# Optimization experiments

Measured on AMD Instinct MI355X. Metric: run time of the kernel, lower is better.

The kernel has to match this reference:

```python
import jax, jax.numpy as jnp
import numpy as np
from jax import lax

SIGMA = 3.0
AP_CUT = 15


def _gauss_kernel(sigma, truncate=4.0):
    r = int(truncate * sigma + 0.5)
    x = np.arange(-r, r + 1, dtype=np.float32)
    k = np.exp(-0.5 * (x / sigma) ** 2)
    return jnp.asarray(k / k.sum()), r

KERN, RAD = _gauss_kernel(SIGMA)


def _smooth(f):
    """Separable Gaussian smoothing; circular on y (DV), replicate on x (AP).
    f: [..., Y, X] -> same shape."""
    lead = f.shape[:-2]
    Y, X = f.shape[-2:]
    g = f.reshape((-1, 1, Y, X))
    g = jnp.pad(g, ((0, 0), (0, 0), (RAD, RAD), (0, 0)), mode='wrap')
    g = jnp.pad(g, ((0, 0), (0, 0), (0, 0), (RAD, RAD)), mode='edge')
    ky = KERN.reshape(1, 1, -1, 1)
    kx = KERN.reshape(1, 1, 1, -1)
    g = lax.conv_general_dilated(g, ky, (1, 1), 'VALID')
    g = lax.conv_general_dilated(g, kx, (1, 1), 'VALID')
    return g.reshape(lead + (Y, X))


def _gradient(f):
    """Covariant gradient: Gaussian smooth then central differences.
    Returns [..., Y, X, 2] with index 0 = d/dy (circular), 1 = d/dx (replicate)."""
    g = _smooth(f)
    dy = 0.5 * (jnp.roll(g, -1, axis=-2) - jnp.roll(g, 1, axis=-2))
    gp = jnp.pad(g, [(0, 0)] * (g.ndim - 1) + [(1, 1)], mode='edge')
    dx = 0.5 * (gp[..., 2:] - gp[..., :-2])
    return jnp.stack([dy, dx], axis=-1)


def _postprocess(f):
    f = f.at[..., :AP_CUT].set(0.0)
    f = f.at[..., -AP_CUT:].set(0.0)
    return _smooth(f)


def setup_inputs() -> dict:
    key = jax.random.key(0)
    k1, k2 = jax.random.split(key)
    Y, X = 1024, 2048
    y = 0.1 * jax.random.normal(k1, (5, Y, X), dtype=jnp.float32)
    v = 0.1 * jax.random.normal(k2, (2, Y, X), dtype=jnp.float32)
    return {"y": y, "v": v}


def reference(y, v):
    Y, X = y.shape[-2:]
    # InputProcessor.transform: split state into 2x2 tensor m and scalar s
    m = y[:4].reshape(2, 2, Y, X)
    s = y[4]

    # get_velocity: left-right symmetrization (flip DV axis, negate y-component)
    v_lr = jnp.flip(v, axis=-2)
    v_lr = v_lr.at[0].multiply(-1.0)
    v = 0.5 * (v + v_lr)

    d1_m = _gradient(m)          # [2,2,Y,X,2]
    d1_s = _gradient(s)          # [Y,X,2]
    d1_v = _gradient(v)          # [2,Y,X,2]

    sdot = -jnp.einsum('iyx,yxi->yx', v, d1_s)

    T = jnp.transpose(d1_v, (0, 3, 1, 2))       # iyxj -> ijyx
    Tt = jnp.transpose(T, (1, 0, 2, 3))
    O = -0.5 * (T - Tt)                         # vorticity
    E = 0.5 * (T + Tt)                          # strain rate

    lhs = jnp.einsum('kyx,ijyxk->ijyx', v, d1_m)
    lhs = lhs + jnp.einsum('ikyx,kjyx->ijyx', O, m)
    lhs = lhs - jnp.einsum('ikyx,kjyx->ijyx', m, O)

    # rhs_eCad reaction terms
    trm = jnp.einsum('kkyx->yx', m)
    trE = jnp.einsum('kkyx->yx', E)
    gamma_dv = jnp.array([[1.0, 0.0], [0.0, 0.0]], dtype=y.dtype)[..., None, None]
    rhs = -(0.11 - 0.099 * s) * m
    rhs = rhs + (0.767 + 0.055 * s) * m * trE
    rhs = rhs + (0.732 - 0.59 * s) * trm * m
    rhs = rhs + (0.069 - 0.048 * s) * trm * gamma_dv

    mdot = _postprocess(-lhs + rhs)
    sdot = _postprocess(sdot)

    # inverse_transform: stack back into 5-channel state derivative
    return jnp.concatenate([mdot.reshape(4, Y, X), sdot[None]], axis=0)
```

## Files before the change

### kernel.cpp

```cpp
#include <hip/hip_runtime.h>
#include <math.h>

#define Y_ 1024
#define X_ 2048
#define YX_ (Y_*X_)
#define RAD_ 12
#define NT_ 25
#define APC_ 15

struct W25 { float w[NT_]; };

__global__ __launch_bounds__(256) void ksmooth_y7(
    const float* __restrict__ yin, const float* __restrict__ vin,
    float* __restrict__ out, W25 W)
{
  const int z  = blockIdx.z;
  const int y0 = blockIdx.y * 8;
  const int xo = (blockIdx.x * 256 + threadIdx.x) * 4;

  float4 acc[8];
#pragma unroll
  for (int j = 0; j < 8; ++j) acc[j] = make_float4(0.f, 0.f, 0.f, 0.f);

#pragma unroll
  for (int t = 0; t < 32; ++t) {
    int r = y0 - RAD_ + t;
    if (r < 0)    r += Y_;
    if (r >= Y_)  r -= Y_;
    float4 val;
    if (z < 5) {
      val = *(const float4*)(yin + z * YX_ + r * X_ + xo);
    } else {
      const int   c   = z - 5;
      const float sgn = (c == 0) ? -1.f : 1.f;
      float4 a = *(const float4*)(vin + c * YX_ + r * X_ + xo);
      float4 b = *(const float4*)(vin + c * YX_ + (Y_ - 1 - r) * X_ + xo);
      val.x = 0.5f * (a.x + sgn * b.x);
      val.y = 0.5f * (a.y + sgn * b.y);
      val.z = 0.5f * (a.z + sgn * b.z);
      val.w = 0.5f * (a.w + sgn * b.w);
    }
#pragma unroll
    for (int j = 0; j < 8; ++j) {
      const int k = t - j;
      if (k >= 0 && k < NT_) {
        const float wk = W.w[k];
        acc[j].x += wk * val.x; acc[j].y += wk * val.y;
        acc[j].z += wk * val.z; acc[j].w += wk * val.w;
      }
    }
  }
#pragma unroll
  for (int j = 0; j < 8; ++j)
    *(float4*)(out + z * YX_ + (y0 + j) * X_ + xo) = acc[j];
}

__global__ __launch_bounds__(256) void ksmooth_y(
    const float* __restrict__ in, float* __restrict__ out, W25 W)
{
  const int z  = blockIdx.z;
  const int y0 = blockIdx.y * 8;
  const int xo = (blockIdx.x * 256 + threadIdx.x) * 4;

  float4 acc[8];
#pragma unroll
  for (int j = 0; j < 8; ++j) acc[j] = make_float4(0.f, 0.f, 0.f, 0.f);

#pragma unroll
  for (int t = 0; t < 32; ++t) {
    int r = y0 - RAD_ + t;
    if (r < 0)    r += Y_;
    if (r >= Y_)  r -= Y_;
    float4 val = *(const float4*)(in + z * YX_ + r * X_ + xo);
#pragma unroll
    for (int j = 0; j < 8; ++j) {
      const int k = t - j;
      if (k >= 0 && k < NT_) {
        const float wk = W.w[k];
        acc[j].x += wk * val.x; acc[j].y += wk * val.y;
        acc[j].z += wk * val.z; acc[j].w += wk * val.w;
      }
    }
  }
#pragma unroll
  for (int j = 0; j < 8; ++j)
    *(float4*)(out + z * YX_ + (y0 + j) * X_ + xo) = acc[j];
}

__global__ __launch_bounds__(256) void ksmooth_x(
    const float* __restrict__ in, float* __restrict__ out, W25 W)
{
  const int z  = blockIdx.z;
  const int yy = blockIdx.y;
  const int x0 = (blockIdx.x * 256 + threadIdx.x) * 4;
  const float* row = in + z * YX_ + yy * X_;

  float buf[28];
  if (x0 >= RAD_ && x0 + 4 + RAD_ <= X_) {
#pragma unroll
    for (int i = 0; i < 7; ++i) {
      float4 t = *(const float4*)(row + x0 - RAD_ + 4 * i);
      buf[4*i+0] = t.x; buf[4*i+1] = t.y; buf[4*i+2] = t.z; buf[4*i+3] = t.w;
    }
  } else {
#pragma unroll
    for (int i = 0; i < 28; ++i) {
      int xx = x0 - RAD_ + i;
      xx = xx < 0 ? 0 : (xx > X_ - 1 ? X_ - 1 : xx);
      buf[i] = row[xx];
    }
  }
  float a0 = 0.f, a1 = 0.f, a2 = 0.f, a3 = 0.f;
#pragma unroll
  for (int t = 0; t < NT_; ++t) {
    const float wk = W.w[t];
    a0 += wk * buf[t + 0];
    a1 += wk * buf[t + 1];
    a2 += wk * buf[t + 2];
    a3 += wk * buf[t + 3];
  }
  *(float4*)(out + z * YX_ + yy * X_ + x0) = make_float4(a0, a1, a2, a3);
}

__global__ __launch_bounds__(256) void kpoint(
    const float* __restrict__ gs,
    const float* __restrict__ yin,
    const float* __restrict__ vin,
    float* __restrict__ out)
{
  const int yy = blockIdx.y;
  const int x0 = (blockIdx.x * 256 + threadIdx.x) * 4;
  const int yu = (yy + 1) & (Y_ - 1);
  const int yd = (yy - 1 + Y_) & (Y_ - 1);

  float dYg[7][4], dXg[7][4];
#pragma unroll
  for (int c = 0; c < 7; ++c) {
    const float* base = gs + c * YX_;
    float4 cc = *(const float4*)(base + yy * X_ + x0);
    float4 uu = *(const float4*)(base + yu * X_ + x0);
    float4 dd = *(const float4*)(base + yd * X_ + x0);
    float L  = (x0 == 0)       ? cc.x : base[yy * X_ + x0 - 1];
    float Rr = (x0 + 4 >= X_)  ? cc.w : base[yy * X_ + x0 + 4];
    dYg[c][0] = 0.5f * (uu.x - dd.x);
    dYg[c][1] = 0.5f * (uu.y - dd.y);
    dYg[c][2] = 0.5f * (uu.z - dd.z);
    dYg[c][3] = 0.5f * (uu.w - dd.w);
    dXg[c][0] = 0.5f * (cc.y - L);
    dXg[c][1] = 0.5f * (cc.z - cc.x);
    dXg[c][2] = 0.5f * (cc.w - cc.y);
    dXg[c][3] = 0.5f * (Rr - cc.z);
  }

  float rm[5][4];
#pragma unroll
  for (int zc = 0; zc < 5; ++zc) {
    float4 t = *(const float4*)(yin + zc * YX_ + yy * X_ + x0);
    rm[zc][0] = t.x; rm[zc][1] = t.y; rm[zc][2] = t.z; rm[zc][3] = t.w;
  }
  float vs0[4], vs1[4];
  {
    float4 a = *(const float4*)(vin + 0 * YX_ + yy * X_ + x0);
    float4 b = *(const float4*)(vin + 0 * YX_ + (Y_ - 1 - yy) * X_ + x0);
    vs0[0] = 0.5f * (a.x - b.x); vs0[1] = 0.5f * (a.y - b.y);
    vs0[2] = 0.5f * (a.z - b.z); vs0[3] = 0.5f * (a.w - b.w);
    float4 c = *(const float4*)(vin + 1 * YX_ + yy * X_ + x0);
    float4 d = *(const float4*)(vin + 1 * YX_ + (Y_ - 1 - yy) * X_ + x0);
    vs1[0] = 0.5f * (c.x + d.x); vs1[1] = 0.5f * (c.y + d.y);
    vs1[2] = 0.5f * (c.z + d.z); vs1[3] = 0.5f * (c.w + d.w);
  }

  float o[5][4];
#pragma unroll
  for (int j = 0; j < 4; ++j) {
    const float m00r = rm[0][j], m01r = rm[1][j], m10r = rm[2][j], m11r = rm[3][j];
    const float sr   = rm[4][j];
    const float v0   = vs0[j], v1 = vs1[j];

    const float w_  = -0.5f * (dXg[5][j] - dYg[6][j]);
    const float trE = dYg[5][j] + dXg[6][j];
    const float trm = m00r + m11r;

    const float adv00 = v0 * dYg[0][j] + v1 * dXg[0][j];
    const float adv01 = v0 * dYg[1][j] + v1 * dXg[1][j];
    const float adv10 = v0 * dYg[2][j] + v1 * dXg[2][j];
    const float adv11 = v0 * dYg[3][j] + v1 * dXg[3][j];

    const float lhs00 = adv00 + w_ * (m10r + m01r);
    const float lhs01 = adv01 + w_ * (m11r - m00r);
    const float lhs10 = adv10 + w_ * (m11r - m00r);
    const float lhs11 = adv11 - w_ * (m01r + m10r);

    const float f  = -(0.11f - 0.099f * sr)
                   + (0.767f + 0.055f * sr) * trE
                   + (0.732f - 0.59f  * sr) * trm;
    const float cd = (0.069f - 0.048f * sr) * trm;

    const float sd = -(v0 * dYg[4][j] + v1 * dXg[4][j]);

    const int   xg   = x0 + j;
    const float mask = (xg < APC_ || xg >= X_ - APC_) ? 0.f : 1.f;
    o[0][j] = mask * (f * m00r + cd - lhs00);
    o[1][j] = mask * (f * m01r      - lhs01);
    o[2][j] = mask * (f * m10r      - lhs10);
    o[3][j] = mask * (f * m11r      - lhs11);
    o[4][j] = mask * sd;
  }
#pragma unroll
  for (int zc = 0; zc < 5; ++zc)
    *(float4*)(out + zc * YX_ + yy * X_ + x0) =
        make_float4(o[zc][0], o[zc][1], o[zc][2], o[zc][3]);
}

extern "C" void kernel_launch(void* const* d_in, const int* in_sizes, int n_in,
                              void* d_out, int out_size, void* d_ws, size_t ws_size,
                              hipStream_t stream)
{
  const float* yin = (const float*)d_in[0];
  const float* vin = (const float*)d_in[1];
  float* out = (float*)d_out;

  float* wsA = (float*)d_ws;
  float* wsB = wsA + 7 * (size_t)YX_;

  W25 W;
  double wd[NT_], s = 0.0;
  for (int i = 0; i < NT_; ++i) {
    double x = i - RAD_;
    wd[i] = exp(-0.5 * (x / 3.0) * (x / 3.0));
    s += wd[i];
  }
  for (int i = 0; i < NT_; ++i) W.w[i] = (float)(wd[i] / s);

  ksmooth_y7<<<dim3(2, 128, 7), 256, 0, stream>>>(yin, vin, wsA, W);
  ksmooth_x <<<dim3(2, 1024, 7), 256, 0, stream>>>(wsA, wsB, W);
  kpoint    <<<dim3(2, 1024, 1), 256, 0, stream>>>(wsB, yin, vin, wsA);
  ksmooth_y <<<dim3(2, 128, 5), 256, 0, stream>>>(wsA, wsB, W);
  ksmooth_x <<<dim3(2, 1024, 5), 256, 0, stream>>>(wsB, out, W);
}
```

Measured before the change: 239.8 us.

## Fuse x-smoothing into gradient and postprocess kernels, folding derivative into filter

Removes the separate x-direction smoothing passes. The x-gradient becomes a single 27-tap derivative-of-Gaussian filter, and the y-gradient applies the x-Gaussian to central differences inside the pointwise kernel. The final smoothing does the x-filter on the fly for each input row before the y-accumulation. The y-smoothing kernel now produces 16 rows per thread instead of 8. Two intermediate 7- and 5-channel round trips through global memory go away, at the cost of redundant x-filter arithmetic per row. Edge columns are zeroed early, which relies on the AP cut masking the replicate-boundary region.

```diff
diff --git a/kernel.cpp b/kernel.cpp
--- a/kernel.cpp
+++ b/kernel.cpp
@@ -6,27 +6,28 @@
 #define YX_ (Y_*X_)
 #define RAD_ 12
 #define NT_ 25
+#define ND_ 27
 #define APC_ 15
+#define PAD_ 16
 
 struct W25 { float w[NT_]; };
+struct D27 { float d[ND_]; };
 
 __global__ __launch_bounds__(256) void ksmooth_y7(
     const float* __restrict__ yin, const float* __restrict__ vin,
     float* __restrict__ out, W25 W)
 {
   const int z  = blockIdx.z;
-  const int y0 = blockIdx.y * 8;
+  const int y0 = blockIdx.y * 16;
   const int xo = (blockIdx.x * 256 + threadIdx.x) * 4;
 
-  float4 acc[8];
-#pragma unroll
-  for (int j = 0; j < 8; ++j) acc[j] = make_float4(0.f, 0.f, 0.f, 0.f);
-
-#pragma unroll
-  for (int t = 0; t < 32; ++t) {
-    int r = y0 - RAD_ + t;
-    if (r < 0)    r += Y_;
-    if (r >= Y_)  r -= Y_;
+  float4 acc[16];
+#pragma unroll
+  for (int j = 0; j < 16; ++j) acc[j] = make_float4(0.f, 0.f, 0.f, 0.f);
+
+#pragma unroll
+  for (int t = 0; t < 40; ++t) {
+    const int r = (y0 - RAD_ + t + Y_) & (Y_ - 1);
     float4 val;
     if (z < 5) {
       val = *(const float4*)(yin + z * YX_ + r * X_ + xo);
@@ -41,7 +42,7 @@
       val.w = 0.5f * (a.w + sgn * b.w);
     }
 #pragma unroll
-    for (int j = 0; j < 8; ++j) {
+    for (int j = 0; j < 16; ++j) {
       const int k = t - j;
       if (k >= 0 && k < NT_) {
         const float wk = W.w[k];
@@ -51,105 +52,66 @@
     }
   }
 #pragma unroll
-  for (int j = 0; j < 8; ++j)
+  for (int j = 0; j < 16; ++j)
     *(float4*)(out + z * YX_ + (y0 + j) * X_ + xo) = acc[j];
 }
 
-__global__ __launch_bounds__(256) void ksmooth_y(
-    const float* __restrict__ in, float* __restrict__ out, W25 W)
-{
-  const int z  = blockIdx.z;
-  const int y0 = blockIdx.y * 8;
-  const int xo = (blockIdx.x * 256 + threadIdx.x) * 4;
-
-  float4 acc[8];
-#pragma unroll
-  for (int j = 0; j < 8; ++j) acc[j] = make_float4(0.f, 0.f, 0.f, 0.f);
-
-#pragma unroll
-  for (int t = 0; t < 32; ++t) {
-    int r = y0 - RAD_ + t;
-    if (r < 0)    r += Y_;
-    if (r >= Y_)  r -= Y_;
-    float4 val = *(const float4*)(in + z * YX_ + r * X_ + xo);
-#pragma unroll
-    for (int j = 0; j < 8; ++j) {
-      const int k = t - j;
-      if (k >= 0 && k < NT_) {
-        const float wk = W.w[k];
-        acc[j].x += wk * val.x; acc[j].y += wk * val.y;
-        acc[j].z += wk * val.z; acc[j].w += wk * val.w;
-      }
-    }
-  }
-#pragma unroll
-  for (int j = 0; j < 8; ++j)
-    *(float4*)(out + z * YX_ + (y0 + j) * X_ + xo) = acc[j];
-}
-
-__global__ __launch_bounds__(256) void ksmooth_x(
-    const float* __restrict__ in, float* __restrict__ out, W25 W)
-{
-  const int z  = blockIdx.z;
+__global__ __launch_bounds__(256) void kgradpoint(
+    const float* __restrict__ gY,
+    const float* __restrict__ yin,
+    const float* __restrict__ vin,
+    float* __restrict__ out,
+    W25 W, D27 D)
+{
   const int yy = blockIdx.y;
   const int x0 = (blockIdx.x * 256 + threadIdx.x) * 4;
-  const float* row = in + z * YX_ + yy * X_;
-
-  float buf[28];
-  if (x0 >= RAD_ && x0 + 4 + RAD_ <= X_) {
-#pragma unroll
-    for (int i = 0; i < 7; ++i) {
-      float4 t = *(const float4*)(row + x0 - RAD_ + 4 * i);
-      buf[4*i+0] = t.x; buf[4*i+1] = t.y; buf[4*i+2] = t.z; buf[4*i+3] = t.w;
-    }
-  } else {
-#pragma unroll
-    for (int i = 0; i < 28; ++i) {
-      int xx = x0 - RAD_ + i;
-      xx = xx < 0 ? 0 : (xx > X_ - 1 ? X_ - 1 : xx);
-      buf[i] = row[xx];
-    }
-  }
-  float a0 = 0.f, a1 = 0.f, a2 = 0.f, a3 = 0.f;
-#pragma unroll
-  for (int t = 0; t < NT_; ++t) {
-    const float wk = W.w[t];
-    a0 += wk * buf[t + 0];
-    a1 += wk * buf[t + 1];
-    a2 += wk * buf[t + 2];
-    a3 += wk * buf[t + 3];
-  }
-  *(float4*)(out + z * YX_ + yy * X_ + x0) = make_float4(a0, a1, a2, a3);
-}
-
-__global__ __launch_bounds__(256) void kpoint(
-    const float* __restrict__ gs,
-    const float* __restrict__ yin,
-    const float* __restrict__ vin,
-    float* __restrict__ out)
-{
-  const int yy = blockIdx.y;
-  const int x0 = (blockIdx.x * 256 + threadIdx.x) * 4;
+
+  if (x0 < RAD_ || x0 > X_ - PAD_) {
+#pragma unroll
+    for (int zc = 0; zc < 5; ++zc)
+      *(float4*)(out + zc * YX_ + yy * X_ + x0) = make_float4(0.f, 0.f, 0.f, 0.f);
+    return;
+  }
+
   const int yu = (yy + 1) & (Y_ - 1);
   const int yd = (yy - 1 + Y_) & (Y_ - 1);
 
   float dYg[7][4], dXg[7][4];
 #pragma unroll
   for (int c = 0; c < 7; ++c) {
-    const float* base = gs + c * YX_;
-    float4 cc = *(const float4*)(base + yy * X_ + x0);
-    float4 uu = *(const float4*)(base + yu * X_ + x0);
-    float4 dd = *(const float4*)(base + yd * X_ + x0);
-    float L  = (x0 == 0)       ? cc.x : base[yy * X_ + x0 - 1];
-    float Rr = (x0 + 4 >= X_)  ? cc.w : base[yy * X_ + x0 + 4];
-    dYg[c][0] = 0.5f * (uu.x - dd.x);
-    dYg[c][1] = 0.5f * (uu.y - dd.y);
-    dYg[c][2] = 0.5f * (uu.z - dd.z);
-    dYg[c][3] = 0.5f * (uu.w - dd.w);
-    dXg[c][0] = 0.5f * (cc.y - L);
-    dXg[c][1] = 0.5f * (cc.z - cc.x);
-    dXg[c][2] = 0.5f * (cc.w - cc.y);
-    dXg[c][3] = 0.5f * (Rr - cc.z);
+    const float* rc = gY + c * YX_ + yy * X_;
+    const float* ru = gY + c * YX_ + yu * X_;
+    const float* rd = gY + c * YX_ + yd * X_;
+
+    float wb[36];
+#pragma unroll
+    for (int i = 0; i < 9; ++i) {
+      float4 t = *(const float4*)(rc + x0 - 16 + 4 * i);
+      wb[4*i+0] = t.x; wb[4*i+1] = t.y; wb[4*i+2] = t.z; wb[4*i+3] = t.w;
+    }
+#pragma unroll
+    for (int j = 0; j < 4; ++j) {
+      float s = 0.f;
+#pragma unroll
+      for (int t = 0; t < ND_; ++t) s += D.d[t] * wb[3 + j + t];
+      dXg[c][j] = s;
+    }
+
+    float db[28];
+#pragma unroll
+    for (int i = 0; i < 7; ++i) {
+      float4 u = *(const float4*)(ru + x0 - 12 + 4 * i);
+      float4 d = *(const float4*)(rd + x0 - 12 + 4 * i);
+      db[4*i+0] = 0.5f * (u.x - d.x); db[4*i+1] = 0.5f * (u.y - d.y);
+      db[4*i+2] = 0.5f * (u.z - d.z); db[4*i+3] = 0.5f * (u.w - d.w);
+    }
+#pragma unroll
+    for (int j = 0; j < 4; ++j) {
+      float s = 0.f;
+#pragma unroll
+      for (int t = 0; t < NT_; ++t) s += W.w[t] * db[j + t];
+      dYg[c][j] = s;
+    }
   }
 
   float rm[5][4];
@@ -181,21 +143,15 @@
     const float trE = dYg[5][j] + dXg[6][j];
     const float trm = m00r + m11r;
 
-    const float adv00 = v0 * dYg[0][j] + v1 * dXg[0][j];
-    const float adv01 = v0 * dYg[1][j] + v1 * dXg[1][j];
-    const float adv10 = v0 * dYg[2][j] + v1 * dXg[2][j];
-    const float adv11 = v0 * dYg[3][j] + v1 * dXg[3][j];
-
-    const float lhs00 = adv00 + w_ * (m10r + m01r);
-    const float lhs01 = adv01 + w_ * (m11r - m00r);
-    const float lhs10 = adv10 + w_ * (m11r - m00r);
-    const float lhs11 = adv11 - w_ * (m01r + m10r);
+    const float lhs00 = v0 * dYg[0][j] + v1 * dXg[0][j] + w_ * (m10r + m01r);
+    const float lhs01 = v0 * dYg[1][j] + v1 * dXg[1][j] + w_ * (m11r - m00r);
+    const float lhs10 = v0 * dYg[2][j] + v1 * dXg[2][j] + w_ * (m11r - m00r);
+    const float lhs11 = v0 * dYg[3][j] + v1 * dXg[3][j] - w_ * (m01r + m10r);
 
     const float f  = -(0.11f - 0.099f * sr)
                    + (0.767f + 0.055f * sr) * trE
                    + (0.732f - 0.59f  * sr) * trm;
     const float cd = (0.069f - 0.048f * sr) * trm;
-
     const float sd = -(v0 * dYg[4][j] + v1 * dXg[4][j]);
 
     const int   xg   = x0 + j;
@@ -212,6 +168,61 @@
         make_float4(o[zc][0], o[zc][1], o[zc][2], o[zc][3]);
 }
 
+__global__ __launch_bounds__(256) void kpost(
+    const float* __restrict__ B, float* __restrict__ out, W25 W)
+{
+  const int z  = blockIdx.z;
+  const int y0 = blockIdx.y * 16;
+  const int xo = (blockIdx.x * 256 + threadIdx.x) * 4;
+  const bool fast = (xo >= RAD_ && xo <= X_ - PAD_);
+
+  float4 acc[16];
+#pragma unroll
+  for (int j = 0; j < 16; ++j) acc[j] = make_float4(0.f, 0.f, 0.f, 0.f);
+
+  for (int t = 0; t < 40; ++t) {
+    const int r = (y0 - RAD_ + t + Y_) & (Y_ - 1);
+    const float* row = B + z * YX_ + r * X_;
+    float xb[28];
+    if (fast) {
+#pragma unroll
+      for (int i = 0; i < 7; ++i) {
+        float4 v = *(const float4*)(row + xo - 12 + 4 * i);
+        xb[4*i+0] = v.x; xb[4*i+1] = v.y; xb[4*i+2] = v.z; xb[4*i+3] = v.w;
+      }
+    } else {
+#pragma unroll
+      for (int i = 0; i < 28; ++i) {
+        const int xx = xo - 12 + i;
+        xb[i] = (xx >= 0 && xx < X_) ? row[xx] : 0.f;
+      }
+    }
+    float4 xs;
+    {
+      float a0 = 0.f, a1 = 0.f, a2 = 0.f, a3 = 0.f;
+#pragma unroll
+      for (int k = 0; k < NT_; ++k) {
+        const float wk = W.w[k];
+        a0 += wk * xb[k + 0]; a1 += wk * xb[k + 1];
+        a2 += wk * xb[k + 2]; a3 += wk * xb[k + 3];
+      }
+      xs = make_float4(a0, a1, a2, a3);
+    }
+#pragma unroll
+    for (int j = 0; j < 16; ++j) {
+      const int k = t - j;
+      if (k >= 0 && k < NT_) {
+        const float wk = W.w[k];
+        acc[j].x += wk * xs.x; acc[j].y += wk * xs.y;
+        acc[j].z += wk * xs.z; acc[j].w += wk * xs.w;
+      }
+    }
+  }
+#pragma unroll
+  for (int j = 0; j < 16; ++j)
+    *(float4*)(out + z * YX_ + (y0 + j) * X_ + xo) = acc[j];
+}
+
 extern "C" void kernel_launch(void* const* d_in, const int* in_sizes, int n_in,
                               void* d_out, int out_size, void* d_ws, size_t ws_size,
                               hipStream_t stream)
@@ -220,21 +231,24 @@
   const float* vin = (const float*)d_in[1];
   float* out = (float*)d_out;
 
-  float* wsA = (float*)d_ws;
-  float* wsB = wsA + 7 * (size_t)YX_;
-
-  W25 W;
+  float* gY = (float*)d_ws + PAD_;
+  float* B  = gY + 7 * (size_t)YX_;
+
+  W25 W; D27 D;
   double wd[NT_], s = 0.0;
   for (int i = 0; i < NT_; ++i) {
-    double x = i - RAD_;
+    const double x = i - RAD_;
     wd[i] = exp(-0.5 * (x / 3.0) * (x / 3.0));
     s += wd[i];
   }
   for (int i = 0; i < NT_; ++i) W.w[i] = (float)(wd[i] / s);
-
-  ksmooth_y7<<<dim3(2, 128, 7), 256, 0, stream>>>(yin, vin, wsA, W);
-  ksmooth_x <<<dim3(2, 1024, 7), 256, 0, stream>>>(wsA, wsB, W);
-  kpoint    <<<dim3(2, 1024, 1), 256, 0, stream>>>(wsB, yin, vin, wsA);
-  ksmooth_y <<<dim3(2, 128, 5), 256, 0, stream>>>(wsA, wsB, W);
-  ksmooth_x <<<dim3(2, 1024, 5), 256, 0, stream>>>(wsB, out, W);
-}
+  for (int t = 0; t < ND_; ++t) {
+    const double a = (t - 2 >= 0 && t - 2 < NT_) ? wd[t - 2] / s : 0.0;
+    const double b = (t < NT_) ? wd[t] / s : 0.0;
+    D.d[t] = (float)(0.5 * (a - b));
+  }
+
+  ksmooth_y7<<<dim3(2,  64, 7), 256, 0, stream>>>(yin, vin, gY, W);
+  kgradpoint<<<dim3(2, 1024, 1), 256, 0, stream>>>(gY, yin, vin, B, W, D);
+  kpost     <<<dim3(2,  64, 5), 256, 0, stream>>>(B, out, W);
+}
```

Measured after the change: 359.8 us. 1.5x slower.
